# Kernel tuning notes

Measured on AMD Instinct MI355X. Metric: run time of the kernel, lower is better.

## Reference

```python
import jax, jax.numpy as jnp
import numpy as np

K = 16

def _pairwise_distance(points):
    # points: (B, N, F) -> (B, N, N)
    r = jnp.sum(points * points, axis=2, keepdims=True)  # (B,N,1)
    m = jnp.einsum('bnf,bmf->bnm', points, points)
    return r - 2.0 * m + jnp.swapaxes(r, 1, 2) + 1e-5

def _block(points, features, W1, b1, W2, b2):
    D = _pairwise_distance(points)
    _, idx = jax.lax.top_k(-D, K + 1)          # (B,N,K+1)
    idx = idx[:, :, 1:]                          # drop self -> (B,N,K)
    neighbors = jax.vmap(lambda f, i: f[i])(features, idx)  # (B,N,K,C)
    center = jnp.broadcast_to(features[:, :, None, :], neighbors.shape)
    edge = jnp.concatenate([neighbors - center, center], axis=-1)  # (B,N,K,2C)
    h = jax.nn.gelu(edge @ W1 + b1, approximate=False)
    h = jax.nn.gelu(h @ W2 + b2, approximate=False)
    return jnp.mean(h, axis=2)  # (B,N,proj)

def setup_inputs() -> dict:
    key = jax.random.key(0)
    ks = jax.random.split(key, 8)
    B, N, C_in, P, F = 64, 512, 32, 64, 3
    s = lambda fan: 1.0 / np.sqrt(fan)
    return {
        'x': jax.random.normal(ks[0], (B, N, C_in), jnp.float32),
        'points': jax.random.normal(ks[1], (B, N, F), jnp.float32),
        'mask': jax.random.randint(ks[2], (B, N, 1), 0, 2).astype(jnp.int32),
        'W1_0': jax.random.normal(ks[3], (2 * C_in, 2 * P), jnp.float32) * s(2 * C_in),
        'b1_0': jnp.zeros((2 * P,), jnp.float32),
        'W2_0': jax.random.normal(ks[4], (2 * P, P), jnp.float32) * s(2 * P),
        'b2_0': jnp.zeros((P,), jnp.float32),
        'W1_1': jax.random.normal(ks[5], (2 * P, 2 * P), jnp.float32) * s(2 * P),
        'b1_1': jnp.zeros((2 * P,), jnp.float32),
        'W2_1': jax.random.normal(ks[6], (2 * P, P), jnp.float32) * s(2 * P),
        'b2_1': jnp.zeros((P,), jnp.float32),
    }

def reference(x, points, mask, W1_0, b1_0, W2_0, b2_0, W1_1, b1_1, W2_1, b2_1):
    mask_f = mask.astype(jnp.float32)
    coord_shift = 999.0 * (mask == 0).astype(jnp.float32)  # (B,N,1)
    feats = _block(coord_shift + points, x, W1_0, b1_0, W2_0, b2_0)
    feats = _block(coord_shift + feats, feats, W1_1, b1_1, W2_1, b2_1)
    return feats * mask_f
```

## Files before the change

### kernel.cpp

```cpp
#include <hip/hip_runtime.h>
#include <math.h>

#define BB 64
#define NN 512
#define KK 16

__device__ __forceinline__ float gelu32(float x) {
    return 0.5f * x * (1.0f + erff(x * 0.70710678118654752440f));
}

#define TAB_N 261
__device__ __forceinline__ double gelu64_tab(double x, const double2* s_tab) {
    double ax = fabs(x);
    if (ax >= 5.74) return x > 0.0 ? x : 0.0;
    double z = ax * 0.70710678118654752440;
    double u = z * 64.0;
    int i = (int)(u + 0.5);
    double zi = (double)i * (1.0 / 64.0);
    double d = z - zi;
    double2 t = s_tab[i];
    double poly = d * (1.0 + d * (-zi + d * ((2.0 * zi * zi - 1.0) * (1.0 / 3.0))));
    double er = t.x + t.y * poly;
    double s = (x > 0.0) ? er : -er;
    return 0.5 * x * (1.0 + s);
}

__global__ void build_tab(double2* __restrict__ g_tab) {
    for (int i = threadIdx.x; i < TAB_N; i += 256) {
        double z = (double)i * (1.0 / 64.0);
        double2 e;
        e.x = erf(z);
        e.y = 1.12837916709551257390 * exp(-z * z);
        g_tab[i] = e;
    }
}

#define SELECT_TOP17(d, lane, OUT_STMT)                                        \
    for (int it = 0; it <= KK; ++it) {                                         \
        double bd = d[0];                                                      \
        int bi = lane;                                                         \
        _Pragma("unroll")                                                      \
        for (int i = 1; i < 8; ++i) {                                          \
            int m = lane + 64 * i;                                             \
            if (d[i] < bd) { bd = d[i]; bi = m; }                              \
        }                                                                      \
        for (int off = 32; off > 0; off >>= 1) {                               \
            double od = __shfl_xor(bd, off, 64);                               \
            int    oi = __shfl_xor(bi, off, 64);                               \
            if (od < bd || (od == bd && oi < bi)) { bd = od; bi = oi; }        \
        }                                                                      \
        const int wl = bi & 63, wsl = bi >> 6;                                 \
        _Pragma("unroll")                                                      \
        for (int i = 0; i < 8; ++i)                                            \
            if (lane == wl && i == wsl) d[i] = 1e300;                          \
        if (it > 0 && lane == 0) { OUT_STMT; }                                 \
    }

__global__ __launch_bounds__(512) void knn1_uv1(const float* __restrict__ points,
                                                const int* __restrict__ mask,
                                                const float* __restrict__ x,
                                                const float* __restrict__ W1,
                                                int uvb,
                                                int* __restrict__ idx_out,
                                                double* __restrict__ U1,
                                                int* __restrict__ cu,
                                                int* __restrict__ nU) {
    __shared__ double sbuf[3 * NN];
    const int tid = threadIdx.x;

    if (blockIdx.x < BB * NN / 8) {
        double (*pts)[NN] = (double (*)[NN])sbuf;
        const int b = blockIdx.x >> 6;
        const int n0 = (blockIdx.x & 63) * 8;
        const int w = tid >> 6, lane = tid & 63;

        for (int e = tid; e < NN; e += 512) {
            double sh = (mask[b * NN + e] == 0) ? 999.0 : 0.0;
            const float* p = points + ((size_t)b * NN + e) * 3;
            pts[0][e] = (double)p[0] + sh;
            pts[1][e] = (double)p[1] + sh;
            pts[2][e] = (double)p[2] + sh;
        }
        __syncthreads();

        const int n = n0 + w;
        if (mask[b * NN + n] == 0) return;
        const double q0 = pts[0][n], q1 = pts[1][n], q2 = pts[2][n];
        double d[8];
        #pragma unroll
        for (int i = 0; i < 8; ++i) {
            int m = lane + 64 * i;
            double d0 = q0 - pts[0][m], d1 = q1 - pts[1][m], d2 = q2 - pts[2][m];
            d[i] = d0 * d0 + d1 * d1 + d2 * d2;
        }

        int* orow = idx_out + (size_t)(b * NN + n) * KK;
        SELECT_TOP17(d, lane, orow[it - 1] = bi)
    } else if (blockIdx.x < BB * NN / 8 + uvb) {
        double (*xs)[32] = (double (*)[32])sbuf;
        const int row0 = (blockIdx.x - BB * NN / 8) * 8;
        if (tid < 256) xs[tid >> 5][tid & 31] = (double)x[(size_t)row0 * 32 + tid];
        __syncthreads();
        const int j = tid & 127;
        const int rr = tid >> 7;
        #pragma unroll
        for (int p = 0; p < 2; ++p) {
            const int r = p * 4 + rr;
            const int row = row0 + r;
            if (mask[row] != 0) {
                double acc = 0.0;
                #pragma unroll 4
                for (int c = 0; c < 32; ++c) acc += xs[r][c] * (double)W1[c * 128 + j];
                U1[(size_t)row * 128 + j] = acc;
            }
        }
    } else {
        __shared__ int wcnt[8], woff[8];
        const int b = blockIdx.x - (BB * NN / 8 + uvb);
        const int w = tid >> 6, lane = tid & 63;
        const int bit = (mask[b * NN + tid] != 0) ? 1 : 0;
        unsigned long long bal = __ballot(bit);
        int pos = __popcll(bal & ((1ull << lane) - 1ull));
        if (lane == 0) wcnt[w] = __popcll(bal);
        __syncthreads();
        if (tid == 0) {
            int acc = 0;
            #pragma unroll
            for (int i = 0; i < 8; ++i) { woff[i] = acc; acc += wcnt[i]; }
            nU[b] = acc;
        }
        __syncthreads();
        if (bit) cu[b * NN + woff[w] + pos] = tid;
    }
}

template<int UV>
__global__ __launch_bounds__(256, 2) void mlp1_f64(const float* __restrict__ x,
                                                   const int* __restrict__ idx,
                                                   const float* __restrict__ W1,
                                                   const float* __restrict__ b1,
                                                   const float* __restrict__ W2,
                                                   const float* __restrict__ b2,
                                                   const float* __restrict__ W1n,
                                                   const double2* __restrict__ g_tab,
                                                   const int* __restrict__ mask,
                                                   const double* __restrict__ U1,
                                                   double* __restrict__ feats_out,
                                                   double* __restrict__ rm,
                                                   float* __restrict__ U2) {
    const int C = 32;
    __shared__ double2 s_tab[TAB_N];
    __shared__ double ctr[32];
    __shared__ double H1[KK][128];
    __shared__ double part[4][64];
    __shared__ float f_row[64];
    const int swz = ((blockIdx.x & 7) << 12) + (blockIdx.x >> 3);
    const int b = swz >> 9;
    const int bn = swz;
    const int tid = threadIdx.x;

    if (mask[bn] == 0) return;

    for (int i = tid; i < TAB_N; i += 256) s_tab[i] = g_tab[i];
    if (tid < C) ctr[tid] = (double)x[(size_t)bn * C + tid];
    __syncthreads();

    if constexpr (UV) {
        const int j = tid & 127;
        const int kb = (tid >> 7) * 8;
        double tn = (double)b1[j];
        #pragma unroll 4
        for (int c = 0; c < C; ++c)
            tn += ctr[c] * ((double)W1[(C + c) * 128 + j] - (double)W1[c * 128 + j]);
        #pragma unroll
        for (int kk = 0; kk < 8; ++kk) {
            int m = idx[bn * KK + kb + kk];
            double v = U1[(size_t)(b * NN + m) * 128 + j] + tn;
            H1[kb + kk][j] = gelu64_tab(v, s_tab);
        }
    } else {
        __shared__ double edg[KK][32];
        for (int e = tid; e < KK * C; e += 256) {
            int k = e >> 5, c = e & 31;
            int m = idx[bn * KK + k];
            edg[k][c] = (double)x[((size_t)b * NN + m) * C + c] - ctr[c];
        }
        __syncthreads();
        const int j = tid & 127;
        const int kb = (tid >> 7) * 8;
        double cterm = (double)b1[j];
        #pragma unroll 2
        for (int c = 0; c < C; ++c) cterm += ctr[c] * (double)W1[(C + c) * 128 + j];
        double acc[8];
        #pragma unroll
        for (int kk = 0; kk < 8; ++kk) acc[kk] = cterm;
        #pragma unroll 2
        for (int c = 0; c < C; ++c) {
            double w = (double)W1[c * 128 + j];
            #pragma unroll
            for (int kk = 0; kk < 8; ++kk) acc[kk] += edg[kb + kk][c] * w;
        }
        #pragma unroll
        for (int kk = 0; kk < 8; ++kk) H1[kb + kk][j] = gelu64_tab(acc[kk], s_tab);
    }
    __syncthreads();

    {
        const int j = tid & 63;
        const int g = tid >> 6;
        const int kb = g * 4;
        double acc[4];
        #pragma unroll
        for (int kk = 0; kk < 4; ++kk) acc[kk] = (double)b2[j];
        #pragma unroll 2
        for (int c = 0; c < 128; c += 2) {
            double w0 = (double)W2[c * 64 + j];
            double w1 = (double)W2[(c + 1) * 64 + j];
            double2 h0 = *(const double2*)&H1[kb + 0][c];
            double2 h1 = *(const double2*)&H1[kb + 1][c];
            double2 h2 = *(const double2*)&H1[kb + 2][c];
            double2 h3 = *(const double2*)&H1[kb + 3][c];
            acc[0] += h0.x * w0; acc[0] += h0.y * w1;
            acc[1] += h1.x * w0; acc[1] += h1.y * w1;
            acc[2] += h2.x * w0; acc[2] += h2.y * w1;
            acc[3] += h3.x * w0; acc[3] += h3.y * w1;
        }
        double s = 0.0;
        #pragma unroll
        for (int kk = 0; kk < 4; ++kk) s += gelu64_tab(acc[kk], s_tab);
        part[g][j] = s;
    }
    __syncthreads();

    if (tid < 64) {
        double s = (part[0][tid] + part[1][tid] + part[2][tid] + part[3][tid]) * 0.0625;
        feats_out[(size_t)bn * 64 + tid] = s;
        f_row[tid] = (float)s;
        double s2 = s * s;
        for (int off = 32; off > 0; off >>= 1) s2 += __shfl_xor(s2, off, 64);
        if (tid == 0) rm[bn] = s2;
    }
    if constexpr (UV) {
        __syncthreads();
        if (tid < 128) {
            float acc = 0.0f;
            #pragma unroll 4
            for (int c = 0; c < 64; ++c) acc += f_row[c] * W1n[c * 128 + tid];
            U2[(size_t)bn * 128 + tid] = acc;
        }
    }
}

__global__ __launch_bounds__(512) void knn2(const double* __restrict__ feats,
                                            const int* __restrict__ mask,
                                            const double* __restrict__ rm,
                                            const int* __restrict__ cu,
                                            const int* __restrict__ nU,
                                            int* __restrict__ idx_out) {
    __shared__ double tileT[64][65];
    __shared__ double qsh[8][64];
    __shared__ double qrn[8];
    __shared__ int cI[NN];
    __shared__ int s_nU;
    const int bid = ((blockIdx.x & 7) << 9) + (blockIdx.x >> 3);
    const int b = bid >> 6;
    const int n0 = (bid & 63) * 8;
    const int tid = threadIdx.x;
    const int w = tid >> 6, lane = tid & 63;
    const int n = n0 + w;
    const int qm = mask[b * NN + n];

    if (tid == 0) s_nU = nU[b];
    for (int e = tid; e < NN; e += 512) cI[e] = cu[b * NN + e];
    qsh[w][lane] = feats[(size_t)(b * NN + n) * 64 + lane];
    if (lane == 0) qrn[w] = rm[b * NN + n];
    __syncthreads();

    const int nUl = s_nU;
    const int ntiles = (nUl + 63) >> 6;

    double d[8];
    #pragma unroll
    for (int t = 0; t < 8; ++t) {
        d[t] = 1e300;
        if (t < ntiles) {
            #pragma unroll
            for (int i = 0; i < 8; ++i) {
                int e = tid + 512 * i;
                int f = e & 63, c = e >> 6;
                int slot = t * 64 + c;
                if (slot < nUl)
                    tileT[f][c] = feats[(size_t)(b * NN + cI[slot]) * 64 + f];
            }
            __syncthreads();
            int slot = t * 64 + lane;
            if (qm && slot < nUl) {
                double a0 = 0.0, a1 = 0.0, a2 = 0.0, a3 = 0.0;
                for (int f = 0; f < 64; f += 4) {
                    a0 += qsh[w][f + 0] * tileT[f + 0][lane];
                    a1 += qsh[w][f + 1] * tileT[f + 1][lane];
                    a2 += qsh[w][f + 2] * tileT[f + 2][lane];
                    a3 += qsh[w][f + 3] * tileT[f + 3][lane];
                }
                double dot = (a0 + a1) + (a2 + a3);
                d[t] = qrn[w] + rm[b * NN + cI[slot]] - 2.0 * dot + 1e-5;
            }
            __syncthreads();
        }
    }

    if (qm) {
        int* orow = idx_out + (size_t)(b * NN + n) * KK;
        SELECT_TOP17(d, lane, orow[it - 1] = cI[bi])
    }
}

template<int UV>
__global__ __launch_bounds__(256, 2) void mlp2_f32(const double* __restrict__ feats,
                                                   const int* __restrict__ idx,
                                                   const float* __restrict__ W1,
                                                   const float* __restrict__ b1,
                                                   const float* __restrict__ W2,
                                                   const float* __restrict__ b2,
                                                   const int* __restrict__ mask,
                                                   const float* __restrict__ U2,
                                                   float* __restrict__ out) {
    const int C = 64;
    __shared__ float ctr[64];
    __shared__ float H1[KK][128];
    __shared__ float part[4][64];
    const int swz = ((blockIdx.x & 7) << 12) + (blockIdx.x >> 3);
    const int b = swz >> 9;
    const int bn = swz;
    const int tid = threadIdx.x;

    if (mask[bn] == 0) {
        if (tid < 64) out[(size_t)bn * 64 + tid] = 0.0f;
        return;
    }

    if (tid < C) ctr[tid] = (float)feats[(size_t)bn * C + tid];
    __syncthreads();

    if constexpr (UV) {
        const int j = tid & 127;
        const int kb = (tid >> 7) * 8;
        float tn = b1[j];
        #pragma unroll 4
        for (int c = 0; c < C; ++c)
            tn += ctr[c] * (W1[(C + c) * 128 + j] - W1[c * 128 + j]);
        #pragma unroll
        for (int kk = 0; kk < 8; ++kk) {
            int m = idx[bn * KK + kb + kk];
            H1[kb + kk][j] = gelu32(U2[(size_t)(b * NN + m) * 128 + j] + tn);
        }
    } else {
        __shared__ float edg[KK][64];
        for (int e = tid; e < KK * C; e += 256) {
            int k = e >> 6, c = e & 63;
            int m = idx[bn * KK + k];
            edg[k][c] = (float)feats[((size_t)b * NN + m) * C + c] - ctr[c];
        }
        __syncthreads();
        const int j = tid & 127;
        const int kb = (tid >> 7) * 8;
        float cterm = b1[j];
        #pragma unroll 2
        for (int c = 0; c < C; ++c) cterm += ctr[c] * W1[(C + c) * 128 + j];
        float acc[8];
        #pragma unroll
        for (int kk = 0; kk < 8; ++kk) acc[kk] = cterm;
        #pragma unroll 2
        for (int c = 0; c < C; ++c) {
            float w = W1[c * 128 + j];
            #pragma unroll
            for (int kk = 0; kk < 8; ++kk) acc[kk] += edg[kb + kk][c] * w;
        }
        #pragma unroll
        for (int kk = 0; kk < 8; ++kk) H1[kb + kk][j] = gelu32(acc[kk]);
    }
    __syncthreads();

    {
        const int j = tid & 63;
        const int g = tid >> 6;
        const int kb = g * 4;
        float acc[4];
        #pragma unroll
        for (int kk = 0; kk < 4; ++kk) acc[kk] = b2[j];
        #pragma unroll 2
        for (int c = 0; c < 128; c += 4) {
            float w0 = W2[(c + 0) * 64 + j];
            float w1 = W2[(c + 1) * 64 + j];
            float w2 = W2[(c + 2) * 64 + j];
            float w3 = W2[(c + 3) * 64 + j];
            #pragma unroll
            for (int kk = 0; kk < 4; ++kk) {
                float4 h = *(const float4*)&H1[kb + kk][c];
                acc[kk] += h.x * w0; acc[kk] += h.y * w1;
                acc[kk] += h.z * w2; acc[kk] += h.w * w3;
            }
        }
        float s = 0.0f;
        #pragma unroll
        for (int kk = 0; kk < 4; ++kk) s += gelu32(acc[kk]);
        part[g][j] = s;
    }
    __syncthreads();

    if (tid < 64) {
        float s = (part[0][tid] + part[1][tid] + part[2][tid] + part[3][tid]) * 0.0625f;
        out[(size_t)bn * 64 + tid] = s;
    }
}

extern "C" void kernel_launch(void* const* d_in, const int* in_sizes, int n_in,
                              void* d_out, int out_size, void* d_ws, size_t ws_size,
                              hipStream_t stream) {
    const float* x      = (const float*)d_in[0];
    const float* points = (const float*)d_in[1];
    const int*   mask   = (const int*)d_in[2];
    const float* W1_0 = (const float*)d_in[3];
    const float* b1_0 = (const float*)d_in[4];
    const float* W2_0 = (const float*)d_in[5];
    const float* b2_0 = (const float*)d_in[6];
    const float* W1_1 = (const float*)d_in[7];
    const float* b1_1 = (const float*)d_in[8];
    const float* W2_1 = (const float*)d_in[9];
    const float* b2_1 = (const float*)d_in[10];

    char* ws = (char*)d_ws;
    const size_t off_tab   = 0;
    const size_t off_idx   = 16384;
    const size_t off_feats = off_idx + 2097152;
    const size_t off_rm    = off_feats + 16777216;
    const size_t off_cu    = off_rm + 262144;
    const size_t off_nu    = off_cu + 131072;
    const size_t off_u1    = off_nu + 4096;
    const size_t off_u2    = off_u1 + 33554432;
    const size_t need      = off_u2 + 16777216;

    double2* tab    = (double2*)(ws + off_tab);
    int*     idx    = (int*)(ws + off_idx);
    double*  feats1 = (double*)(ws + off_feats);
    double*  rm     = (double*)(ws + off_rm);
    int*     cu     = (int*)(ws + off_cu);
    int*     nU     = (int*)(ws + off_nu);
    double*  U1     = (double*)(ws + off_u1);
    float*   U2     = (float*)(ws + off_u2);

    const int use_uv = (ws_size >= need) ? 1 : 0;
    const int uvb = use_uv ? BB * NN / 8 : 0;
    const int grid1 = BB * NN / 8 + uvb + BB;

    build_tab<<<1, 256, 0, stream>>>(tab);
    knn1_uv1<<<grid1, 512, 0, stream>>>(points, mask, x, W1_0, uvb, idx, U1, cu, nU);
    if (use_uv) {
        mlp1_f64<1><<<BB * NN, 256, 0, stream>>>(x, idx, W1_0, b1_0, W2_0, b2_0, W1_1,
                                                 tab, mask, U1, feats1, rm, U2);
        knn2<<<BB * NN / 8, 512, 0, stream>>>(feats1, mask, rm, cu, nU, idx);
        mlp2_f32<1><<<BB * NN, 256, 0, stream>>>(feats1, idx, W1_1, b1_1, W2_1, b2_1,
                                                 mask, U2, (float*)d_out);
    } else {
        mlp1_f64<0><<<BB * NN, 256, 0, stream>>>(x, idx, W1_0, b1_0, W2_0, b2_0, W1_1,
                                                 tab, mask, U1, feats1, rm, U2);
        knn2<<<BB * NN / 8, 512, 0, stream>>>(feats1, mask, rm, cu, nU, idx);
        mlp2_f32<0><<<BB * NN, 256, 0, stream>>>(feats1, idx, W1_1, b1_1, W2_1, b2_1,
                                                 mask, U2, (float*)d_out);
    }
}
```

Baseline: 644.2 us.

## Fold erf table build into knn kernel, read table from global, retile second GEMM

Moves the erf lookup-table construction into an extra block of the first kNN kernel, removing one kernel launch. mlp1 now reads the table straight from global/L1 instead of copying it into shared memory for every block. Both MLP kernels retile the second-layer GEMM so each thread computes a 2x2 block (two rows, two output columns) instead of four rows of one column, which cuts shared-memory H1 loads per FMA. The cost is that the table lookups become scattered global reads, and the partial-sum shared buffer doubles in size.

```diff
diff --git a/kernel.cpp b/kernel.cpp
--- a/kernel.cpp
+++ b/kernel.cpp
@@ -10,7 +10,7 @@
 }
 
 #define TAB_N 261
-__device__ __forceinline__ double gelu64_tab(double x, const double2* s_tab) {
+__device__ __forceinline__ double gelu64_tab(double x, const double2* __restrict__ tab) {
     double ax = fabs(x);
     if (ax >= 5.74) return x > 0.0 ? x : 0.0;
     double z = ax * 0.70710678118654752440;
@@ -18,21 +18,11 @@
     int i = (int)(u + 0.5);
     double zi = (double)i * (1.0 / 64.0);
     double d = z - zi;
-    double2 t = s_tab[i];
+    double2 t = tab[i];
     double poly = d * (1.0 + d * (-zi + d * ((2.0 * zi * zi - 1.0) * (1.0 / 3.0))));
     double er = t.x + t.y * poly;
     double s = (x > 0.0) ? er : -er;
     return 0.5 * x * (1.0 + s);
-}
-
-__global__ void build_tab(double2* __restrict__ g_tab) {
-    for (int i = threadIdx.x; i < TAB_N; i += 256) {
-        double z = (double)i * (1.0 / 64.0);
-        double2 e;
-        e.x = erf(z);
-        e.y = 1.12837916709551257390 * exp(-z * z);
-        g_tab[i] = e;
-    }
 }
 
 #define SELECT_TOP17(d, lane, OUT_STMT)                                        \
@@ -64,7 +54,8 @@
                                                 int* __restrict__ idx_out,
                                                 double* __restrict__ U1,
                                                 int* __restrict__ cu,
-                                                int* __restrict__ nU) {
+                                                int* __restrict__ nU,
+                                                double2* __restrict__ g_tab) {
     __shared__ double sbuf[3 * NN];
     const int tid = threadIdx.x;
 
@@ -114,7 +105,7 @@
                 U1[(size_t)row * 128 + j] = acc;
             }
         }
-    } else {
+    } else if (blockIdx.x < BB * NN / 8 + uvb + BB) {
         __shared__ int wcnt[8], woff[8];
         const int b = blockIdx.x - (BB * NN / 8 + uvb);
         const int w = tid >> 6, lane = tid & 63;
@@ -131,6 +122,14 @@
         }
         __syncthreads();
         if (bit) cu[b * NN + woff[w] + pos] = tid;
+    } else {
+        for (int i = tid; i < TAB_N; i += 512) {
+            double z = (double)i * (1.0 / 64.0);
+            double2 e;
+            e.x = erf(z);
+            e.y = 1.12837916709551257390 * exp(-z * z);
+            g_tab[i] = e;
+        }
     }
 }
 
@@ -149,10 +148,9 @@
                                                    double* __restrict__ rm,
                                                    float* __restrict__ U2) {
     const int C = 32;
-    __shared__ double2 s_tab[TAB_N];
     __shared__ double ctr[32];
-    __shared__ double H1[KK][128];
-    __shared__ double part[4][64];
+    __shared__ __align__(16) double H1[KK][128];
+    __shared__ double part2[4][2][64];
     __shared__ float f_row[64];
     const int swz = ((blockIdx.x & 7) << 12) + (blockIdx.x >> 3);
     const int b = swz >> 9;
@@ -161,7 +159,6 @@
 
     if (mask[bn] == 0) return;
 
-    for (int i = tid; i < TAB_N; i += 256) s_tab[i] = g_tab[i];
     if (tid < C) ctr[tid] = (double)x[(size_t)bn * C + tid];
     __syncthreads();
 
@@ -176,7 +173,7 @@
         for (int kk = 0; kk < 8; ++kk) {
             int m = idx[bn * KK + kb + kk];
             double v = U1[(size_t)(b * NN + m) * 128 + j] + tn;
-            H1[kb + kk][j] = gelu64_tab(v, s_tab);
+            H1[kb + kk][j] = gelu64_tab(v, g_tab);
         }
     } else {
         __shared__ double edg[KK][32];
@@ -201,39 +198,42 @@
             for (int kk = 0; kk < 8; ++kk) acc[kk] += edg[kb + kk][c] * w;
         }
         #pragma unroll
-        for (int kk = 0; kk < 8; ++kk) H1[kb + kk][j] = gelu64_tab(acc[kk], s_tab);
+        for (int kk = 0; kk < 8; ++kk) H1[kb + kk][j] = gelu64_tab(acc[kk], g_tab);
     }
     __syncthreads();
 
     {
-        const int j = tid & 63;
-        const int g = tid >> 6;
-        const int kb = g * 4;
-        double acc[4];
-        #pragma unroll
-        for (int kk = 0; kk < 4; ++kk) acc[kk] = (double)b2[j];
+        const int w = tid >> 6;
+        const int l = tid & 63;
+        const int jlo = l & 31;
+        const int kh = l >> 5;
+        const int r0 = w * 4 + kh * 2;
+        double a00 = (double)b2[jlo], a01 = (double)b2[jlo + 32];
+        double a10 = a00, a11 = a01;
         #pragma unroll 2
         for (int c = 0; c < 128; c += 2) {
-            double w0 = (double)W2[c * 64 + j];
-            double w1 = (double)W2[(c + 1) * 64 + j];
-            double2 h0 = *(const double2*)&H1[kb + 0][c];
-            double2 h1 = *(const double2*)&H1[kb + 1][c];
-            double2 h2 = *(const double2*)&H1[kb + 2][c];
-            double2 h3 = *(const double2*)&H1[kb + 3][c];
-            acc[0] += h0.x * w0; acc[0] += h0.y * w1;
-            acc[1] += h1.x * w0; acc[1] += h1.y * w1;
-            acc[2] += h2.x * w0; acc[2] += h2.y * w1;
-            acc[3] += h3.x * w0; acc[3] += h3.y * w1;
-        }
+            double2 h0 = *(const double2*)&H1[r0][c];
+            double2 h1 = *(const double2*)&H1[r0 + 1][c];
+            double w00 = (double)W2[c * 64 + jlo];
+            double w01 = (double)W2[c * 64 + jlo + 32];
+            double w10 = (double)W2[(c + 1) * 64 + jlo];
+            double w11 = (double)W2[(c + 1) * 64 + jlo + 32];
+            a00 += h0.x * w00; a00 += h0.y * w10;
+            a01 += h0.x * w01; a01 += h0.y * w11;
+            a10 += h1.x * w00; a10 += h1.y * w10;
+            a11 += h1.x * w01; a11 += h1.y * w11;
+        }
+        part2[w][kh][jlo]      = gelu64_tab(a00, g_tab) + gelu64_tab(a10, g_tab);
+        part2[w][kh][jlo + 32] = gelu64_tab(a01, g_tab) + gelu64_tab(a11, g_tab);
+    }
+    __syncthreads();
+
+    if (tid < 64) {
         double s = 0.0;
         #pragma unroll
-        for (int kk = 0; kk < 4; ++kk) s += gelu64_tab(acc[kk], s_tab);
-        part[g][j] = s;
-    }
-    __syncthreads();
-
-    if (tid < 64) {
-        double s = (part[0][tid] + part[1][tid] + part[2][tid] + part[3][tid]) * 0.0625;
+        for (int w8 = 0; w8 < 4; ++w8)
+            s += part2[w8][0][tid] + part2[w8][1][tid];
+        s *= 0.0625;
         feats_out[(size_t)bn * 64 + tid] = s;
         f_row[tid] = (float)s;
         double s2 = s * s;
@@ -327,8 +327,8 @@
                                                    float* __restrict__ out) {
     const int C = 64;
     __shared__ float ctr[64];
-    __shared__ float H1[KK][128];
-    __shared__ float part[4][64];
+    __shared__ __align__(16) float H1[KK][128];
+    __shared__ float part2[4][2][64];
     const int swz = ((blockIdx.x & 7) << 12) + (blockIdx.x >> 3);
     const int b = swz >> 9;
     const int bn = swz;
@@ -382,35 +382,37 @@
     __syncthreads();
 
     {
-        const int j = tid & 63;
-        const int g = tid >> 6;
-        const int kb = g * 4;
-        float acc[4];
-        #pragma unroll
-        for (int kk = 0; kk < 4; ++kk) acc[kk] = b2[j];
+        const int w = tid >> 6;
+        const int l = tid & 63;
+        const int jlo = l & 31;
+        const int kh = l >> 5;
+        const int r0 = w * 4 + kh * 2;
+        float a00 = b2[jlo], a01 = b2[jlo + 32];
+        float a10 = a00, a11 = a01;
         #pragma unroll 2
         for (int c = 0; c < 128; c += 4) {
-            float w0 = W2[(c + 0) * 64 + j];
-            float w1 = W2[(c + 1) * 64 + j];
-            float w2 = W2[(c + 2) * 64 + j];
-            float w3 = W2[(c + 3) * 64 + j];
-            #pragma unroll
-            for (int kk = 0; kk < 4; ++kk) {
-                float4 h = *(const float4*)&H1[kb + kk][c];
-                acc[kk] += h.x * w0; acc[kk] += h.y * w1;
-                acc[kk] += h.z * w2; acc[kk] += h.w * w3;
-            }
-        }
+            float4 h0 = *(const float4*)&H1[r0][c];
+            float4 h1 = *(const float4*)&H1[r0 + 1][c];
+            float w0a = W2[(c + 0) * 64 + jlo], w0b = W2[(c + 0) * 64 + jlo + 32];
+            float w1a = W2[(c + 1) * 64 + jlo], w1b = W2[(c + 1) * 64 + jlo + 32];
+            float w2a = W2[(c + 2) * 64 + jlo], w2b = W2[(c + 2) * 64 + jlo + 32];
+            float w3a = W2[(c + 3) * 64 + jlo], w3b = W2[(c + 3) * 64 + jlo + 32];
+            a00 += h0.x * w0a; a00 += h0.y * w1a; a00 += h0.z * w2a; a00 += h0.w * w3a;
+            a01 += h0.x * w0b; a01 += h0.y * w1b; a01 += h0.z * w2b; a01 += h0.w * w3b;
+            a10 += h1.x * w0a; a10 += h1.y * w1a; a10 += h1.z * w2a; a10 += h1.w * w3a;
+            a11 += h1.x * w0b; a11 += h1.y * w1b; a11 += h1.z * w2b; a11 += h1.w * w3b;
+        }
+        part2[w][kh][jlo]      = gelu32(a00) + gelu32(a10);
+        part2[w][kh][jlo + 32] = gelu32(a01) + gelu32(a11);
+    }
+    __syncthreads();
+
+    if (tid < 64) {
         float s = 0.0f;
         #pragma unroll
-        for (int kk = 0; kk < 4; ++kk) s += gelu32(acc[kk]);
-        part[g][j] = s;
-    }
-    __syncthreads();
-
-    if (tid < 64) {
-        float s = (part[0][tid] + part[1][tid] + part[2][tid] + part[3][tid]) * 0.0625f;
-        out[(size_t)bn * 64 + tid] = s;
+        for (int w8 = 0; w8 < 4; ++w8)
+            s += part2[w8][0][tid] + part2[w8][1][tid];
+        out[(size_t)bn * 64 + tid] = s * 0.0625f;
     }
 }
 
@@ -451,10 +453,9 @@
 
     const int use_uv = (ws_size >= need) ? 1 : 0;
     const int uvb = use_uv ? BB * NN / 8 : 0;
-    const int grid1 = BB * NN / 8 + uvb + BB;
-
-    build_tab<<<1, 256, 0, stream>>>(tab);
-    knn1_uv1<<<grid1, 512, 0, stream>>>(points, mask, x, W1_0, uvb, idx, U1, cu, nU);
+    const int grid1 = BB * NN / 8 + uvb + BB + 1;
+
+    knn1_uv1<<<grid1, 512, 0, stream>>>(points, mask, x, W1_0, uvb, idx, U1, cu, nU, tab);
     if (use_uv) {
         mlp1_f64<1><<<BB * NN, 256, 0, stream>>>(x, idx, W1_0, b1_0, W2_0, b2_0, W1_1,
                                                  tab, mask, U1, feats1, rm, U2);
```

After: 696.1 us. +8.0%, slower.

## Fold table build into knn launch and pre-pack W2 as double2 for 2x2 register tiling

Applied to the files above, without the earlier changes.

Removes the separate build_tab launch by adding two extra blocks to the knn1 kernel, one building the erf table and one repacking W2_0 into a double-precision interleaved layout. The layer-1 second matmul now has each thread compute a 2-row by 2-column tile from the pre-converted double2 weights, so there are fewer float-to-double conversions and global weight loads per FMA. Partial sums go into a larger shared buffer that is reduced across both halves. The cost is one extra 64 KB workspace buffer, and because build_tab no longer runs as its own launch, mlp1 depends on the knn kernel finishing both new blocks.

```diff
diff --git a/kernel.cpp b/kernel.cpp
--- a/kernel.cpp
+++ b/kernel.cpp
@@ -23,16 +23,6 @@
     double er = t.x + t.y * poly;
     double s = (x > 0.0) ? er : -er;
     return 0.5 * x * (1.0 + s);
-}
-
-__global__ void build_tab(double2* __restrict__ g_tab) {
-    for (int i = threadIdx.x; i < TAB_N; i += 256) {
-        double z = (double)i * (1.0 / 64.0);
-        double2 e;
-        e.x = erf(z);
-        e.y = 1.12837916709551257390 * exp(-z * z);
-        g_tab[i] = e;
-    }
 }
 
 #define SELECT_TOP17(d, lane, OUT_STMT)                                        \
@@ -60,11 +50,14 @@
                                                 const int* __restrict__ mask,
                                                 const float* __restrict__ x,
                                                 const float* __restrict__ W1,
+                                                const float* __restrict__ W2,
                                                 int uvb,
                                                 int* __restrict__ idx_out,
                                                 double* __restrict__ U1,
                                                 int* __restrict__ cu,
-                                                int* __restrict__ nU) {
+                                                int* __restrict__ nU,
+                                                double2* __restrict__ g_tab,
+                                                double2* __restrict__ w2p) {
     __shared__ double sbuf[3 * NN];
     const int tid = threadIdx.x;
 
@@ -114,7 +107,7 @@
                 U1[(size_t)row * 128 + j] = acc;
             }
         }
-    } else {
+    } else if (blockIdx.x < BB * NN / 8 + uvb + BB) {
         __shared__ int wcnt[8], woff[8];
         const int b = blockIdx.x - (BB * NN / 8 + uvb);
         const int w = tid >> 6, lane = tid & 63;
@@ -131,6 +124,22 @@
         }
         __syncthreads();
         if (bit) cu[b * NN + woff[w] + pos] = tid;
+    } else if (blockIdx.x < BB * NN / 8 + uvb + BB + 1) {
+        for (int i = tid; i < TAB_N; i += 512) {
+            double z = (double)i * (1.0 / 64.0);
+            double2 e;
+            e.x = erf(z);
+            e.y = 1.12837916709551257390 * exp(-z * z);
+            g_tab[i] = e;
+        }
+    } else {
+        for (int e = tid; e < 128 * 32; e += 512) {
+            int c = e >> 5, jlo = e & 31;
+            double2 v;
+            v.x = (double)W2[c * 64 + jlo];
+            v.y = (double)W2[c * 64 + jlo + 32];
+            w2p[e] = v;
+        }
     }
 }
 
@@ -139,20 +148,21 @@
                                                    const int* __restrict__ idx,
                                                    const float* __restrict__ W1,
                                                    const float* __restrict__ b1,
-                                                   const float* __restrict__ W2,
                                                    const float* __restrict__ b2,
                                                    const float* __restrict__ W1n,
                                                    const double2* __restrict__ g_tab,
+                                                   const double2* __restrict__ w2p,
                                                    const int* __restrict__ mask,
                                                    const double* __restrict__ U1,
+                                                   const float* __restrict__ W2f,
                                                    double* __restrict__ feats_out,
                                                    double* __restrict__ rm,
                                                    float* __restrict__ U2) {
     const int C = 32;
     __shared__ double2 s_tab[TAB_N];
     __shared__ double ctr[32];
-    __shared__ double H1[KK][128];
-    __shared__ double part[4][64];
+    __shared__ __align__(16) double H1[KK][128];
+    __shared__ double part2[4][2][64];
     __shared__ float f_row[64];
     const int swz = ((blockIdx.x & 7) << 12) + (blockIdx.x >> 3);
     const int b = swz >> 9;
@@ -205,21 +215,42 @@
     }
     __syncthreads();
 
-    {
+    if constexpr (UV) {
+        const int w = tid >> 6;
+        const int l = tid & 63;
+        const int jlo = l & 31;
+        const int kh = l >> 5;
+        const int r0 = w * 4 + kh * 2;
+        double a00 = (double)b2[jlo], a01 = (double)b2[jlo + 32];
+        double a10 = a00, a11 = a01;
+        #pragma unroll 2
+        for (int c = 0; c < 128; c += 2) {
+            double2 h0 = *(const double2*)&H1[r0][c];
+            double2 h1 = *(const double2*)&H1[r0 + 1][c];
+            double2 wp0 = w2p[c * 32 + jlo];
+            double2 wp1 = w2p[(c + 1) * 32 + jlo];
+            a00 += h0.x * wp0.x; a00 += h0.y * wp1.x;
+            a01 += h0.x * wp0.y; a01 += h0.y * wp1.y;
+            a10 += h1.x * wp0.x; a10 += h1.y * wp1.x;
+            a11 += h1.x * wp0.y; a11 += h1.y * wp1.y;
+        }
+        part2[w][kh][jlo]      = gelu64_tab(a00, s_tab) + gelu64_tab(a10, s_tab);
+        part2[w][kh][jlo + 32] = gelu64_tab(a01, s_tab) + gelu64_tab(a11, s_tab);
+    } else {
         const int j = tid & 63;
         const int g = tid >> 6;
-        const int kb = g * 4;
+        const int kb2 = g * 4;
         double acc[4];
         #pragma unroll
         for (int kk = 0; kk < 4; ++kk) acc[kk] = (double)b2[j];
         #pragma unroll 2
         for (int c = 0; c < 128; c += 2) {
-            double w0 = (double)W2[c * 64 + j];
-            double w1 = (double)W2[(c + 1) * 64 + j];
-            double2 h0 = *(const double2*)&H1[kb + 0][c];
-            double2 h1 = *(const double2*)&H1[kb + 1][c];
-            double2 h2 = *(const double2*)&H1[kb + 2][c];
-            double2 h3 = *(const double2*)&H1[kb + 3][c];
+            double w0 = (double)W2f[c * 64 + j];
+            double w1 = (double)W2f[(c + 1) * 64 + j];
+            double2 h0 = *(const double2*)&H1[kb2 + 0][c];
+            double2 h1 = *(const double2*)&H1[kb2 + 1][c];
+            double2 h2 = *(const double2*)&H1[kb2 + 2][c];
+            double2 h3 = *(const double2*)&H1[kb2 + 3][c];
             acc[0] += h0.x * w0; acc[0] += h0.y * w1;
             acc[1] += h1.x * w0; acc[1] += h1.y * w1;
             acc[2] += h2.x * w0; acc[2] += h2.y * w1;
@@ -228,12 +259,22 @@
         double s = 0.0;
         #pragma unroll
         for (int kk = 0; kk < 4; ++kk) s += gelu64_tab(acc[kk], s_tab);
-        part[g][j] = s;
+        part2[g][0][j] = s;
+        if (tid < 64) part2[0][1][tid] = 0.0;
     }
     __syncthreads();
 
     if (tid < 64) {
-        double s = (part[0][tid] + part[1][tid] + part[2][tid] + part[3][tid]) * 0.0625;
+        double s = 0.0;
+        if constexpr (UV) {
+            #pragma unroll
+            for (int w8 = 0; w8 < 4; ++w8)
+                s += part2[w8][0][tid] + part2[w8][1][tid];
+        } else {
+            #pragma unroll
+            for (int w8 = 0; w8 < 4; ++w8) s += part2[w8][0][tid];
+        }
+        s *= 0.0625;
         feats_out[(size_t)bn * 64 + tid] = s;
         f_row[tid] = (float)s;
         double s2 = s * s;
@@ -327,7 +368,7 @@
                                                    float* __restrict__ out) {
     const int C = 64;
     __shared__ float ctr[64];
-    __shared__ float H1[KK][128];
+    __shared__ __align__(16) float H1[KK][128];
     __shared__ float part[4][64];
     const int swz = ((blockIdx.x & 7) << 12) + (blockIdx.x >> 3);
     const int b = swz >> 9;
@@ -436,7 +477,8 @@
     const size_t off_rm    = off_feats + 16777216;
     const size_t off_cu    = off_rm + 262144;
     const size_t off_nu    = off_cu + 131072;
-    const size_t off_u1    = off_nu + 4096;
+    const size_t off_w2p   = off_nu + 4096;
+    const size_t off_u1    = off_w2p + 65536;
     const size_t off_u2    = off_u1 + 33554432;
     const size_t need      = off_u2 + 16777216;
 
@@ -446,24 +488,27 @@
     double*  rm     = (double*)(ws + off_rm);
     int*     cu     = (int*)(ws + off_cu);
     int*     nU     = (int*)(ws + off_nu);
+    double2* w2p    = (double2*)(ws + off_w2p);
     double*  U1     = (double*)(ws + off_u1);
     float*   U2     = (float*)(ws + off_u2);
 
     const int use_uv = (ws_size >= need) ? 1 : 0;
     const int uvb = use_uv ? BB * NN / 8 : 0;
-    const int grid1 = BB * NN / 8 + uvb + BB;
-
-    build_tab<<<1, 256, 0, stream>>>(tab);
-    knn1_uv1<<<grid1, 512, 0, stream>>>(points, mask, x, W1_0, uvb, idx, U1, cu, nU);
+    const int grid1 = BB * NN / 8 + uvb + BB + 2;
+
+    knn1_uv1<<<grid1, 512, 0, stream>>>(points, mask, x, W1_0, W2_0, uvb, idx, U1,
+                                        cu, nU, tab, w2p);
     if (use_uv) {
-        mlp1_f64<1><<<BB * NN, 256, 0, stream>>>(x, idx, W1_0, b1_0, W2_0, b2_0, W1_1,
-                                                 tab, mask, U1, feats1, rm, U2);
+        mlp1_f64<1><<<BB * NN, 256, 0, stream>>>(x, idx, W1_0, b1_0, b2_0, W1_1,
+                                                 tab, w2p, mask, U1, W2_0,
+                                                 feats1, rm, U2);
         knn2<<<BB * NN / 8, 512, 0, stream>>>(feats1, mask, rm, cu, nU, idx);
         mlp2_f32<1><<<BB * NN, 256, 0, stream>>>(feats1, idx, W1_1, b1_1, W2_1, b2_1,
                                                  mask, U2, (float*)d_out);
     } else {
-        mlp1_f64<0><<<BB * NN, 256, 0, stream>>>(x, idx, W1_0, b1_0, W2_0, b2_0, W1_1,
-                                                 tab, mask, U1, feats1, rm, U2);
+        mlp1_f64<0><<<BB * NN, 256, 0, stream>>>(x, idx, W1_0, b1_0, b2_0, W1_1,
+                                                 tab, w2p, mask, U1, W2_0,
+                                                 feats1, rm, U2);
         knn2<<<BB * NN / 8, 512, 0, stream>>>(feats1, mask, rm, cu, nU, idx);
         mlp2_f32<0><<<BB * NN, 256, 0, stream>>>(feats1, idx, W1_1, b1_1, W2_1, b2_1,
                                                  mask, U2, (float*)d_out);
```

After: 740.5 us. 1.15x slower.
